# Performance work log

Hardware: AMD Instinct MI355X
Metric: run time of the kernel (lower is better)

The kernel has to match this reference:

```python
import jax, jax.numpy as jnp
import numpy as np

V, E, H, L = 32000, 256, 512, 2
B, T, S = 64, 64, 64


def setup_inputs() -> dict:
    key = jax.random.key(0)
    ks = jax.random.split(key, 20)
    p = lambda k, shape: (0.02 * jax.random.normal(k, shape)).astype(jnp.float32)
    return {
        "X": jax.random.randint(ks[0], (B, T), 0, V),
        "enc_outputs": jax.random.normal(ks[1], (B, S, H), dtype=jnp.float32),
        "hidden_state": jax.random.normal(ks[2], (L, B, H), dtype=jnp.float32),
        "enc_valid_lens": jax.random.randint(ks[3], (B,), 1, S + 1),
        "emb": p(ks[4], (V, E)),
        "Wq": p(ks[5], (H, H)),
        "Wk": p(ks[6], (H, H)),
        "wv": p(ks[7], (H,)),
        "W_ih0": p(ks[8], (3 * H, E + H)),
        "W_hh0": p(ks[9], (3 * H, H)),
        "b_ih0": p(ks[10], (3 * H,)),
        "b_hh0": p(ks[11], (3 * H,)),
        "W_ih1": p(ks[12], (3 * H, H)),
        "W_hh1": p(ks[13], (3 * H, H)),
        "b_ih1": p(ks[14], (3 * H,)),
        "b_hh1": p(ks[15], (3 * H,)),
        "dense_W": p(ks[16], (V, H)),
        "dense_b": p(ks[17], (V,)),
    }


def _gru_cell(x, h, W_ih, W_hh, b_ih, b_hh):
    gi = x @ W_ih.T + b_ih            # [B, 3H]
    gh = h @ W_hh.T + b_hh            # [B, 3H]
    i_r, i_z, i_n = jnp.split(gi, 3, axis=-1)
    h_r, h_z, h_n = jnp.split(gh, 3, axis=-1)
    r = jax.nn.sigmoid(i_r + h_r)
    z = jax.nn.sigmoid(i_z + h_z)
    n = jnp.tanh(i_n + r * h_n)
    return (1.0 - z) * n + z * h


def reference(X, enc_outputs, hidden_state, enc_valid_lens, emb, Wq, Wk, wv,
              W_ih0, W_hh0, b_ih0, b_hh0, W_ih1, W_hh1, b_ih1, b_hh1,
              dense_W, dense_b):
    # token embeddings, time-major: [T, B, E]
    x_seq = jnp.transpose(emb[X], (1, 0, 2))
    keys_proj = jnp.einsum('bsh,kh->bsk', enc_outputs, Wk)  # precompute W_k(K)
    valid_mask = jnp.arange(S)[None, :] < enc_valid_lens[:, None]  # [B, S]

    def step(h, x_t):
        q = h[-1] @ Wq.T                                     # [B, H]
        feat = jnp.tanh(q[:, None, :] + keys_proj)           # [B, S, H]
        scores = feat @ wv                                   # [B, S]
        attn = jax.nn.softmax(jnp.where(valid_mask, scores, -1e6), axis=-1)
        context = jnp.einsum('bs,bsh->bh', attn, enc_outputs)
        inp = jnp.concatenate([context, x_t], axis=-1)       # [B, H+E]
        h0 = _gru_cell(inp, h[0], W_ih0, W_hh0, b_ih0, b_hh0)
        h1 = _gru_cell(h0, h[1], W_ih1, W_hh1, b_ih1, b_hh1)
        return jnp.stack([h0, h1]), h1

    h_final, outs = jax.lax.scan(step, hidden_state, x_seq)  # outs: [T, B, H]
    logits = outs @ dense_W.T + dense_b                      # [T, B, V]
    return jnp.transpose(logits, (1, 0, 2))                  # [B, T, V]
```

## Files before the change

### kernel.cpp

```cpp
#include <hip/hip_runtime.h>
#include <hip/hip_bf16.h>
#include <hip/hip_fp16.h>

#define VV 32000
#define EE 256
#define HH 512
#define BB 64
#define TT 64
#define SS 64
#define G3 1536
#define NGRU 256
#define STU 16384

typedef __attribute__((ext_vector_type(8))) short bf16x8;
typedef __attribute__((ext_vector_type(4))) float f32x4;
typedef _Float16 half2v __attribute__((ext_vector_type(2)));

__device__ __forceinline__ half2v bch(unsigned u) { return __builtin_bit_cast(half2v, u); }

__device__ __forceinline__ void async16(void* lds, const void* g) {
  __builtin_amdgcn_global_load_lds((const __attribute__((address_space(1))) void*)g,
                                   (__attribute__((address_space(3))) void*)lds, 16, 0, 0);
}

__device__ __forceinline__ float sigmoid_fast(float x) {
  return 1.0f / (1.0f + __expf(-x));
}
__device__ __forceinline__ float tanh_fast(float x) {
  x = fminf(fmaxf(x, -15.f), 15.f);
  float e = __expf(2.f * x);
  return (e - 1.f) / (e + 1.f);
}
__device__ __forceinline__ float2 unpackh2(unsigned u) {
  __half2 h = *reinterpret_cast<__half2*>(&u);
  return __half22float2(h);
}
__device__ __forceinline__ unsigned packh2(float x, float y) {
  __half2 h = __floats2half2_rn(x, y);
  return *reinterpret_cast<unsigned*>(&h);
}
__device__ __forceinline__ unsigned packh2w(float x, float y) {
  half2v h; h[0] = (_Float16)x; h[1] = (_Float16)y;
  return __builtin_bit_cast(unsigned, h);
}

__device__ __forceinline__ void stg_sc(float* p, float v) {
  asm volatile("global_store_dword %0, %1, off sc0 sc1" :: "v"(p), "v"(v) : "memory");
}
__device__ __forceinline__ void stg_scu(unsigned* p, unsigned v) {
  asm volatile("global_store_dword %0, %1, off sc0 sc1" :: "v"(p), "v"(v) : "memory");
}
__device__ __forceinline__ void stg_scu2(unsigned* p, uint2 v) {
  asm volatile("global_store_dwordx2 %0, %1, off sc0 sc1" :: "v"(p), "v"(v) : "memory");
}
__device__ __forceinline__ void stg_sci(int* p, int v) {
  asm volatile("global_store_dword %0, %1, off sc0 sc1" :: "v"(p), "v"(v) : "memory");
}
__device__ __forceinline__ int ld_agent(const int* p) {
  return __hip_atomic_load(p, __ATOMIC_RELAXED, __HIP_MEMORY_SCOPE_AGENT);
}

template <int NBK>
__device__ __forceinline__ void gbar(int* flags, int* go, int phase) {
  __syncthreads();
  if (blockIdx.x == NBK - 1) {
    if (threadIdx.x < 64) {
      const int l = threadIdx.x;
      if (l == 0) stg_sci(&flags[NBK - 1], phase);
      for (;;) {
        bool ok = true;
#pragma unroll
        for (int g = 0; g < NBK / 64; ++g) ok &= (ld_agent(&flags[l + 64 * g]) >= phase);
        if (__all(ok)) break;
        __builtin_amdgcn_s_sleep(1);
      }
      if (l == 0) stg_sci(go, phase);
    }
  } else {
    if (threadIdx.x == 0) {
      stg_sci(&flags[blockIdx.x], phase);
      while (ld_agent(go) < phase) __builtin_amdgcn_s_sleep(1);
    }
  }
  __syncthreads();
}

__global__ __launch_bounds__(256) void transpose_kernel(float* __restrict__ dst,
                                                        const float* __restrict__ src,
                                                        int R, int C, int ld, int off) {
  __shared__ float tile[32][33];
  int c0 = blockIdx.x * 32, r0 = blockIdx.y * 32;
  int x = threadIdx.x, y = threadIdx.y;
  for (int i = y; i < 32; i += 8) tile[i][x] = src[(size_t)(r0 + i) * ld + off + c0 + x];
  __syncthreads();
  for (int i = y; i < 32; i += 8) dst[(size_t)(c0 + i) * R + r0 + x] = tile[x][i];
}

__global__ __launch_bounds__(256) void cast_kernel(const float* __restrict__ src,
                                                   __hip_bfloat16* __restrict__ dst, int n) {
  for (int i = blockIdx.x * blockDim.x + threadIdx.x; i < n; i += gridDim.x * blockDim.x)
    dst[i] = __float2bfloat16(src[i]);
}

__global__ __launch_bounds__(256) void hspack_kernel(const float* __restrict__ hs,
                                                     unsigned* __restrict__ h0u,
                                                     unsigned* __restrict__ h1u) {
  int i = blockIdx.x * 256 + threadIdx.x;
  int layer = i >> 14, r = i & 16383;
  int b = r >> 8, kp = r & 255;
  const float* src = hs + (size_t)layer * BB * HH + (size_t)b * HH + 2 * kp;
  unsigned u = packh2(src[0], src[1]);
  (layer ? h1u : h0u)[(kp >> 1) * 128 + 2 * b + (kp & 1)] = u;
}

__global__ __launch_bounds__(256) void gemm32_kernel(const float* __restrict__ A,
                                                     const int* __restrict__ Xtb,
                                                     const float* __restrict__ Bk,
                                                     const float* __restrict__ bias,
                                                     float* __restrict__ C,
                                                     int N, int K, int ldb, int tbmaj) {
  __shared__ float Xs[32][65];
  __shared__ float Ws[32][129];
  __shared__ int toks[64];
  int m0 = blockIdx.x * 64, n0 = blockIdx.y * 128;
  int tid = threadIdx.x;
  if (tid < 64) {
    int m = m0 + tid;
    toks[tid] = Xtb ? Xtb[(m & 63) * TT + (m >> 6)] : m;
  }
  __syncthreads();
  float acc[4][8];
#pragma unroll
  for (int i = 0; i < 4; ++i)
#pragma unroll
    for (int j = 0; j < 8; ++j) acc[i][j] = 0.f;
  int mi = (tid >> 4) * 4;
  int ni = (tid & 15) * 8;
  for (int kc = 0; kc < K; kc += 32) {
#pragma unroll
    for (int i = 0; i < 16; ++i) {
      int idx = tid + i * 256;
      int kk = idx >> 7, nn = idx & 127;
      Ws[kk][nn] = Bk[(size_t)(kc + kk) * ldb + n0 + nn];
    }
#pragma unroll
    for (int i = 0; i < 8; ++i) {
      int idx = tid + i * 256;
      int mm = idx >> 5, kk = idx & 31;
      Xs[kk][mm] = A[(size_t)toks[mm] * K + kc + kk];
    }
    __syncthreads();
#pragma unroll
    for (int k = 0; k < 32; ++k) {
      float xv[4], wv[8];
#pragma unroll
      for (int i = 0; i < 4; ++i) xv[i] = Xs[k][mi + i];
#pragma unroll
      for (int j = 0; j < 8; ++j) wv[j] = Ws[k][ni + j];
#pragma unroll
      for (int i = 0; i < 4; ++i)
#pragma unroll
        for (int j = 0; j < 8; ++j) acc[i][j] += xv[i] * wv[j];
    }
    __syncthreads();
  }
#pragma unroll
  for (int i = 0; i < 4; ++i) {
    int m = m0 + mi + i;
#pragma unroll
    for (int j = 0; j < 8; ++j) {
      int n = n0 + ni + j;
      float v = acc[i][j] + (bias ? bias[n] : 0.f);
      if (tbmaj) C[((size_t)(m >> 6) * N + n) * BB + (m & 63)] = v;
      else       C[(size_t)m * N + n] = v;
    }
  }
}

struct RecArgs {
  const float *Wq, *W_ih0, *W_hh0, *W_ih1, *W_hh1;
  const float *b_hh0, *b_ih1, *b_hh1;
  const float *gixT, *keysp, *enc, *wv;
  const int* vlen;
  const unsigned *h0i, *h1i;
  float *qS;
  unsigned *ctxS, *h0S, *h1S;
  int *flags, *go;
  __hip_bfloat16* outsb;
};

__device__ __forceinline__ void accum6(const unsigned* __restrict__ xu, int xkp0,
                                       const unsigned (*__restrict__ WL)[8], int wkp0,
                                       int nkp, int b, float s[6]) {
#pragma unroll 4
  for (int i = 0; i < nkp; i += 2) {
    uint2 xv = *(const uint2*)(xu + ((xkp0 + i) >> 1) * 128 + 2 * b);
    half2v x0 = bch(xv.x), x1 = bch(xv.y);
    const unsigned* w0 = WL[wkp0 + i];
    const unsigned* w1 = WL[wkp0 + i + 1];
#pragma unroll
    for (int g = 0; g < 6; ++g) {
      s[g] = __builtin_amdgcn_fdot2(bch(w0[g]), x0, s[g], false);
      s[g] = __builtin_amdgcn_fdot2(bch(w1[g]), x1, s[g], false);
    }
  }
}

template <bool HOIST, int NBK>
__global__ __launch_bounds__(512, 4) void recurrent_kernel(RecArgs a) {
  const int blk = blockIdx.x, tid = threadIdx.x;
  const int w = tid >> 6, lane = tid & 63;
  const bool isGru = HOIST ? (blk < NGRU) : true;
  const bool isAttn = HOIST ? (blk >= NGRU) : (blk < BB);
  const int battn = HOIST ? (blk - NGRU) : blk;
  const int j0 = 2 * blk;

  __shared__ __align__(16) unsigned WLh[2][512][8];
  __shared__ __align__(16) unsigned QLh[256][2];
  __shared__ float redW[6][8][64];
  __shared__ float redH0s[6][64], redH1s[6][64];
  __shared__ float sQ[HH], sWV[HH], sCt[HH], sAttn[SS];

  if (isGru) {
    for (int idx = tid; idx < 2 * 3072; idx += 512) {
      int layer = idx / 3072;
      int rem = idx - layer * 3072;
      int kp = rem / 6, g = rem - kp * 6;
      int gate = g >> 1, jj = g & 1;
      int row = gate * 512 + j0 + jj;
      float w0, w1;
      if (layer == 0) {
        if (kp < 256) { w0 = a.W_ih0[(size_t)row * 768 + 2 * kp];
                        w1 = a.W_ih0[(size_t)row * 768 + 2 * kp + 1]; }
        else          { w0 = a.W_hh0[(size_t)row * 512 + 2 * (kp - 256)];
                        w1 = a.W_hh0[(size_t)row * 512 + 2 * (kp - 256) + 1]; }
      } else {
        if (kp < 256) { w0 = a.W_ih1[(size_t)row * 512 + 2 * kp];
                        w1 = a.W_ih1[(size_t)row * 512 + 2 * kp + 1]; }
        else          { w0 = a.W_hh1[(size_t)row * 512 + 2 * (kp - 256)];
                        w1 = a.W_hh1[(size_t)row * 512 + 2 * (kp - 256) + 1]; }
      }
      WLh[layer][kp][g] = packh2w(w0, w1);
    }
    {
      int kp = tid >> 1, jj = tid & 1;
      QLh[kp][jj] = packh2w(a.Wq[(size_t)(j0 + jj) * HH + 2 * kp],
                            a.Wq[(size_t)(j0 + jj) * HH + 2 * kp + 1]);
    }
  }
  if (isAttn) sWV[tid] = a.wv[tid];
  const int vl = isAttn ? a.vlen[battn] : 0;
  const int hoff = isGru ? ((blk >> 1) * 128 + (blk & 1)) : 0;
  __syncthreads();

  for (int t = 0; t < TT; ++t) {
    const unsigned* h0p = (t == 0) ? a.h0i : a.h0S + (size_t)(t - 1) * STU;
    const unsigned* h1p = (t == 0) ? a.h1i : a.h1S + (size_t)(t - 1) * STU;
    float* qrowT = a.qS + (size_t)t * BB * HH;
    unsigned* ctxu = a.ctxS + (size_t)t * STU;
    unsigned* h0n  = a.h0S + (size_t)t * STU;
    unsigned* h1n  = a.h1S + (size_t)t * STU;

    if (isGru) {
      float q0 = 0.f, q1 = 0.f;
      const int kp0 = w * 32;
#pragma unroll 4
      for (int i = 0; i < 32; i += 2) {
        uint2 xv = *(const uint2*)(h1p + ((kp0 + i) >> 1) * 128 + 2 * lane);
        half2v x0 = bch(xv.x), x1 = bch(xv.y);
        q0 = __builtin_amdgcn_fdot2(bch(QLh[kp0 + i][0]), x0, q0, false);
        q0 = __builtin_amdgcn_fdot2(bch(QLh[kp0 + i + 1][0]), x1, q0, false);
        q1 = __builtin_amdgcn_fdot2(bch(QLh[kp0 + i][1]), x0, q1, false);
        q1 = __builtin_amdgcn_fdot2(bch(QLh[kp0 + i + 1][1]), x1, q1, false);
      }
      redW[0][w][lane] = q0; redW[1][w][lane] = q1;
      __syncthreads();
      if (tid < 64) {
        int b = tid;
        float v0 = 0.f, v1 = 0.f;
#pragma unroll
        for (int q = 0; q < 8; ++q) { v0 += redW[0][q][b]; v1 += redW[1][q][b]; }
        stg_sc(&qrowT[(size_t)b * HH + j0], v0);
        stg_sc(&qrowT[(size_t)b * HH + j0 + 1], v1);
      }
    }
    gbar<NBK>(a.flags, a.go, t * 4 + 1);

    if (HOIST && isGru) {
      float s[6] = {0, 0, 0, 0, 0, 0};
      const int layer = (w >= 4) ? 1 : 0;
      const unsigned* xp = layer ? h1p : h0p;
      const int c = (w & 3) * 64;
      accum6(xp, c, WLh[layer], 256 + c, 64, lane, s);
#pragma unroll
      for (int g = 0; g < 6; ++g) redW[g][w][lane] = s[g];
      __syncthreads();
      if (tid < 128) {
        int b = tid & 63, jj = tid >> 6;
#pragma unroll
        for (int g = 0; g < 3; ++g) {
          int sl = 2 * g + jj;
          redH0s[sl][b] = redW[sl][0][b] + redW[sl][1][b] + redW[sl][2][b] + redW[sl][3][b];
          redH1s[sl][b] = redW[sl][4][b] + redW[sl][5][b] + redW[sl][6][b] + redW[sl][7][b];
        }
      }
    } else if (isAttn) {
      const int b = battn;
      sQ[tid] = qrowT[(size_t)b * HH + tid];
      __syncthreads();
      for (int s = w; s < SS; s += 8) {
        const float* kp = a.keysp + ((size_t)b * SS + s) * HH;
        float p = 0.f;
#pragma unroll
        for (int h = lane; h < HH; h += 64)
          p += tanh_fast(sQ[h] + kp[h]) * sWV[h];
#pragma unroll
        for (int off = 32; off > 0; off >>= 1) p += __shfl_down(p, off);
        if (lane == 0) sAttn[s] = (s < vl) ? p : -1e6f;
      }
      __syncthreads();
      if (w == 0) {
        float v = sAttn[lane];
        float mx = v;
        for (int off = 32; off > 0; off >>= 1) mx = fmaxf(mx, __shfl_xor(mx, off));
        float e = __expf(v - mx);
        float sm = e;
        for (int off = 32; off > 0; off >>= 1) sm += __shfl_xor(sm, off);
        sAttn[lane] = e / sm;
      }
      __syncthreads();
      {
        float c = 0.f;
#pragma unroll 8
        for (int s = 0; s < SS; ++s) c += sAttn[s] * a.enc[((size_t)b * SS + s) * HH + tid];
        sCt[tid] = c;
      }
      __syncthreads();
      if (tid < 128) {
        uint2 v;
        v.x = packh2(sCt[4 * tid], sCt[4 * tid + 1]);
        v.y = packh2(sCt[4 * tid + 2], sCt[4 * tid + 3]);
        stg_scu2(&ctxu[tid * 128 + 2 * b], v);
      }
    }
    gbar<NBK>(a.flags, a.go, t * 4 + 2);

    if (isGru) {
      float gr0, gz0, gn0, gr1, gz1, gn1;
      unsigned holdu = 0;
      if (tid < 64) {
        const int b = tid;
        const float* gx = a.gixT + (size_t)t * G3 * BB;
        gr0 = gx[(size_t)(j0)*BB + b];          gr1 = gx[(size_t)(j0 + 1) * BB + b];
        gz0 = gx[(size_t)(j0 + 512) * BB + b];  gz1 = gx[(size_t)(j0 + 513) * BB + b];
        gn0 = gx[(size_t)(j0 + 1024) * BB + b]; gn1 = gx[(size_t)(j0 + 1025) * BB + b];
        holdu = h0p[hoff + 2 * b];
      }
      float s[6] = {0, 0, 0, 0, 0, 0};
      if (HOIST) {
        accum6(ctxu, w * 32, WLh[0], w * 32, 32, lane, s);
      } else {
        const int c = (w & 3) * 64;
        if (w < 4) accum6(ctxu, c, WLh[0], c, 64, lane, s);
        else       accum6(h0p,  c, WLh[0], 256 + c, 64, lane, s);
      }
#pragma unroll
      for (int g = 0; g < 6; ++g) redW[g][w][lane] = s[g];
      __syncthreads();
      if (tid < 64) {
        const int b = tid;
        float2 hold = unpackh2(holdu);
        float hv[2];
#pragma unroll
        for (int jj = 0; jj < 2; ++jj) {
          int j = j0 + jj;
          float Ri = 0, Zi = 0, Ni = 0, Rh = 0, Zh = 0, Nh = 0;
          if (HOIST) {
#pragma unroll
            for (int q = 0; q < 8; ++q) {
              Ri += redW[jj][q][b]; Zi += redW[2 + jj][q][b]; Ni += redW[4 + jj][q][b];
            }
            Rh = redH0s[jj][b]; Zh = redH0s[2 + jj][b]; Nh = redH0s[4 + jj][b];
          } else {
#pragma unroll
            for (int q = 0; q < 4; ++q) {
              Ri += redW[jj][q][b];     Rh += redW[jj][4 + q][b];
              Zi += redW[2 + jj][q][b]; Zh += redW[2 + jj][4 + q][b];
              Ni += redW[4 + jj][q][b]; Nh += redW[4 + jj][4 + q][b];
            }
          }
          float gr = jj ? gr1 : gr0, gz = jj ? gz1 : gz0, gn = jj ? gn1 : gn0;
          float r = sigmoid_fast(gr + Ri + a.b_hh0[j] + Rh);
          float z = sigmoid_fast(gz + Zi + a.b_hh0[j + 512] + Zh);
          float n = tanh_fast(gn + Ni + r * (a.b_hh0[j + 1024] + Nh));
          float ho = jj ? hold.y : hold.x;
          hv[jj] = (1.f - z) * n + z * ho;
        }
        stg_scu(&h0n[hoff + 2 * b], packh2(hv[0], hv[1]));
      }
    }
    gbar<NBK>(a.flags, a.go, t * 4 + 3);

    if (isGru) {
      unsigned holdu = 0;
      if (tid < 64) holdu = h1p[hoff + 2 * tid];
      float s[6] = {0, 0, 0, 0, 0, 0};
      if (HOIST) {
        accum6(h0n, w * 32, WLh[1], w * 32, 32, lane, s);
      } else {
        const int c = (w & 3) * 64;
        if (w < 4) accum6(h0n, c, WLh[1], c, 64, lane, s);
        else       accum6(h1p, c, WLh[1], 256 + c, 64, lane, s);
      }
#pragma unroll
      for (int g = 0; g < 6; ++g) redW[g][w][lane] = s[g];
      __syncthreads();
      if (tid < 64) {
        const int b = tid;
        float2 hold = unpackh2(holdu);
        float hv[2];
#pragma unroll
        for (int jj = 0; jj < 2; ++jj) {
          int j = j0 + jj;
          float Ri = 0, Zi = 0, Ni = 0, Rh = 0, Zh = 0, Nh = 0;
          if (HOIST) {
#pragma unroll
            for (int q = 0; q < 8; ++q) {
              Ri += redW[jj][q][b]; Zi += redW[2 + jj][q][b]; Ni += redW[4 + jj][q][b];
            }
            Rh = redH1s[jj][b]; Zh = redH1s[2 + jj][b]; Nh = redH1s[4 + jj][b];
          } else {
#pragma unroll
            for (int q = 0; q < 4; ++q) {
              Ri += redW[jj][q][b];     Rh += redW[jj][4 + q][b];
              Zi += redW[2 + jj][q][b]; Zh += redW[2 + jj][4 + q][b];
              Ni += redW[4 + jj][q][b]; Nh += redW[4 + jj][4 + q][b];
            }
          }
          float r = sigmoid_fast(a.b_ih1[j] + Ri + a.b_hh1[j] + Rh);
          float z = sigmoid_fast(a.b_ih1[j + 512] + Zi + a.b_hh1[j + 512] + Zh);
          float n = tanh_fast(a.b_ih1[j + 1024] + Ni + r * (a.b_hh1[j + 1024] + Nh));
          float ho = jj ? hold.y : hold.x;
          hv[jj] = (1.f - z) * n + z * ho;
          a.outsb[((size_t)t * BB + b) * HH + j] = __float2bfloat16(hv[jj]);
        }
        stg_scu(&h1n[hoff + 2 * b], packh2(hv[0], hv[1]));
      }
    }
    gbar<NBK>(a.flags, a.go, t * 4 + 4);
  }
}

__global__ __launch_bounds__(256) void dense_kernel(const __hip_bfloat16* __restrict__ A,
                                                    const __hip_bfloat16* __restrict__ Bt,
                                                    const float* __restrict__ bias,
                                                    float* __restrict__ out) {
  __shared__ __align__(16) short As[128 * 64];
  __shared__ __align__(16) short Bs[128 * 64];
  int mt = blockIdx.x;
  int nt = blockIdx.y;
  int tid = threadIdx.x;
  int w = tid >> 6, lane = tid & 63;
  int wm = w >> 1, wn = w & 1;
  f32x4 acc[4][4];
#pragma unroll
  for (int m = 0; m < 4; ++m)
#pragma unroll
    for (int n = 0; n < 4; ++n) acc[m][n] = (f32x4)0.f;

  const short* Ag = (const short*)A + (size_t)(mt * 128) * 512;
  const short* Bg = (const short*)Bt + (size_t)(nt * 128) * 512;

  for (int kt = 0; kt < 8; ++kt) {
    int k0 = kt * 64;
#pragma unroll
    for (int c = 0; c < 4; ++c) {
      int chunk = w * 4 + c;
      int row = chunk * 8 + (lane >> 3);
      int col = (lane & 7) * 8;
      async16(As + chunk * 512, Ag + (size_t)row * 512 + k0 + col);
      async16(Bs + chunk * 512, Bg + (size_t)row * 512 + k0 + col);
    }
    __syncthreads();
#pragma unroll
    for (int kk = 0; kk < 2; ++kk) {
      int krow = kk * 32 + (lane >> 4) * 8;
      bf16x8 af[4], bf[4];
#pragma unroll
      for (int m = 0; m < 4; ++m) {
        int r = wm * 64 + m * 16 + (lane & 15);
        af[m] = *(const bf16x8*)&As[r * 64 + krow];
      }
#pragma unroll
      for (int n = 0; n < 4; ++n) {
        int r = wn * 64 + n * 16 + (lane & 15);
        bf[n] = *(const bf16x8*)&Bs[r * 64 + krow];
      }
#pragma unroll
      for (int m = 0; m < 4; ++m)
#pragma unroll
        for (int n = 0; n < 4; ++n)
          acc[m][n] = __builtin_amdgcn_mfma_f32_16x16x32_bf16(af[m], bf[n], acc[m][n], 0, 0, 0);
    }
    __syncthreads();
  }
#pragma unroll
  for (int m = 0; m < 4; ++m) {
    int rbase = mt * 128 + wm * 64 + m * 16 + (lane >> 4) * 4;
#pragma unroll
    for (int n = 0; n < 4; ++n) {
      int v = nt * 128 + wn * 64 + n * 16 + (lane & 15);
      float bv = bias[v];
#pragma unroll
      for (int r = 0; r < 4; ++r) {
        int mi = rbase + r;
        size_t off = (size_t)(mi & 63) * (TT * VV) + (size_t)(mi >> 6) * VV + v;
        out[off] = acc[m][n][r] + bv;
      }
    }
  }
}

extern "C" void kernel_launch(void* const* d_in, const int* in_sizes, int n_in,
                              void* d_out, int out_size, void* d_ws, size_t ws_size,
                              hipStream_t stream) {
  const int*   X     = (const int*)d_in[0];
  const float* enc   = (const float*)d_in[1];
  const float* hs    = (const float*)d_in[2];
  const int*   vlen  = (const int*)d_in[3];
  const float* emb   = (const float*)d_in[4];
  const float* Wq    = (const float*)d_in[5];
  const float* Wk    = (const float*)d_in[6];
  const float* wv    = (const float*)d_in[7];
  const float* W_ih0 = (const float*)d_in[8];
  const float* W_hh0 = (const float*)d_in[9];
  const float* b_ih0 = (const float*)d_in[10];
  const float* b_hh0 = (const float*)d_in[11];
  const float* W_ih1 = (const float*)d_in[12];
  const float* W_hh1 = (const float*)d_in[13];
  const float* b_ih1 = (const float*)d_in[14];
  const float* b_hh1 = (const float*)d_in[15];
  const float* dW    = (const float*)d_in[16];
  const float* db    = (const float*)d_in[17];
  float* out = (float*)d_out;

  char* wp = (char*)d_ws;
  auto alloc = [&](size_t bytes) { char* p = wp; wp += (bytes + 255) & ~(size_t)255; return p; };
  __hip_bfloat16* dWb   = (__hip_bfloat16*)alloc((size_t)VV * HH * 2);
  __hip_bfloat16* outsb = (__hip_bfloat16*)alloc((size_t)TT * BB * HH * 2);
  float* keysp = (float*)alloc((size_t)BB * SS * HH * 4);
  float* gixT  = (float*)alloc((size_t)TT * G3 * BB * 4);
  float* WkT   = (float*)alloc((size_t)HH * HH * 4);
  float* WT0e  = (float*)alloc((size_t)EE * G3 * 4);
  float* qS    = (float*)alloc((size_t)TT * BB * HH * 4);
  unsigned* h0i  = (unsigned*)alloc((size_t)STU * 4);
  unsigned* h1i  = (unsigned*)alloc((size_t)STU * 4);
  unsigned* ctxS = (unsigned*)alloc((size_t)TT * STU * 4);
  unsigned* h0S  = (unsigned*)alloc((size_t)TT * STU * 4);
  unsigned* h1S  = (unsigned*)alloc((size_t)TT * STU * 4);
  int* flags = (int*)alloc(320 * sizeof(int));
  int* go    = (int*)alloc(64 * sizeof(int));

  hipMemsetAsync(flags, 0, 320 * sizeof(int), stream);
  hipMemsetAsync(go, 0, 64 * sizeof(int), stream);

  dim3 tb(32, 8);
  transpose_kernel<<<dim3(HH / 32, HH / 32), tb, 0, stream>>>(WkT, Wk, HH, HH, HH, 0);
  transpose_kernel<<<dim3(EE / 32, G3 / 32), tb, 0, stream>>>(WT0e, W_ih0, G3, EE, HH + EE, HH);
  cast_kernel<<<2048, 256, 0, stream>>>(dW, dWb, VV * HH);
  hspack_kernel<<<128, 256, 0, stream>>>(hs, h0i, h1i);

  gemm32_kernel<<<dim3(BB * SS / 64, HH / 128), 256, 0, stream>>>(
      enc, nullptr, WkT, nullptr, keysp, HH, HH, HH, 0);
  gemm32_kernel<<<dim3(TT * BB / 64, G3 / 128), 256, 0, stream>>>(
      emb, X, WT0e, b_ih0, gixT, G3, EE, G3, 1);

  RecArgs args;
  args.Wq = Wq; args.W_ih0 = W_ih0; args.W_hh0 = W_hh0; args.W_ih1 = W_ih1; args.W_hh1 = W_hh1;
  args.b_hh0 = b_hh0; args.b_ih1 = b_ih1; args.b_hh1 = b_hh1;
  args.gixT = gixT; args.keysp = keysp; args.enc = enc; args.wv = wv; args.vlen = vlen;
  args.h0i = h0i; args.h1i = h1i;
  args.qS = qS; args.ctxS = ctxS; args.h0S = h0S; args.h1S = h1S;
  args.flags = flags; args.go = go; args.outsb = outsb;
  void* kp[] = {&args};

  int maxb = 0;
  hipError_t qe = hipOccupancyMaxActiveBlocksPerMultiprocessor(
      &maxb, reinterpret_cast<const void*>(recurrent_kernel<true, 320>), 512, 0);
  bool launchedA = false;
  if (qe == hipSuccess && maxb >= 2) {
    hipError_t le = hipLaunchCooperativeKernel(
        reinterpret_cast<void*>(recurrent_kernel<true, 320>),
        dim3(320), dim3(512), kp, 0, stream);
    launchedA = (le == hipSuccess);
  }
  if (!launchedA) {
    hipLaunchCooperativeKernel(
        reinterpret_cast<void*>(recurrent_kernel<false, 256>),
        dim3(256), dim3(512), kp, 0, stream);
  }

  dense_kernel<<<dim3(32, 250), 256, 0, stream>>>(outsb, dWb, db, out);
}
```

Baseline: 2.229 ms.

## Decentralize grid barrier and pack attention keys/encoder outputs to fp16

The grid barrier no longer relays through a master block writing a go flag. Every block now polls all arrival flags directly, removing one global-memory round trip per barrier at the cost of more polling traffic. Separately, the projected keys and the encoder outputs are pre-packed into half2 words by a new kernel. The per-step attention score and context loops then read half the bytes, with some loss of precision on these activations.

```diff
diff --git a/kernel.cpp b/kernel.cpp
--- a/kernel.cpp
+++ b/kernel.cpp
@@ -61,25 +61,17 @@
 }
 
 template <int NBK>
-__device__ __forceinline__ void gbar(int* flags, int* go, int phase) {
+__device__ __forceinline__ void gbar(int* flags, int phase) {
   __syncthreads();
-  if (blockIdx.x == NBK - 1) {
-    if (threadIdx.x < 64) {
-      const int l = threadIdx.x;
-      if (l == 0) stg_sci(&flags[NBK - 1], phase);
-      for (;;) {
-        bool ok = true;
-#pragma unroll
-        for (int g = 0; g < NBK / 64; ++g) ok &= (ld_agent(&flags[l + 64 * g]) >= phase);
-        if (__all(ok)) break;
-        __builtin_amdgcn_s_sleep(1);
-      }
-      if (l == 0) stg_sci(go, phase);
-    }
-  } else {
-    if (threadIdx.x == 0) {
-      stg_sci(&flags[blockIdx.x], phase);
-      while (ld_agent(go) < phase) __builtin_amdgcn_s_sleep(1);
+  if (threadIdx.x < 64) {
+    const int l = threadIdx.x;
+    if (l == 0) stg_sci(&flags[blockIdx.x], phase);
+    for (;;) {
+      bool ok = true;
+#pragma unroll
+      for (int g = 0; g < NBK / 64; ++g) ok &= (ld_agent(&flags[l + 64 * g]) >= phase);
+      if (__all(ok)) break;
+      __builtin_amdgcn_s_sleep(1);
     }
   }
   __syncthreads();
@@ -100,6 +92,12 @@
                                                    __hip_bfloat16* __restrict__ dst, int n) {
   for (int i = blockIdx.x * blockDim.x + threadIdx.x; i < n; i += gridDim.x * blockDim.x)
     dst[i] = __float2bfloat16(src[i]);
+}
+
+__global__ __launch_bounds__(256) void packhalf_kernel(const float* __restrict__ src,
+                                                       unsigned* __restrict__ dst, int npairs) {
+  for (int i = blockIdx.x * blockDim.x + threadIdx.x; i < npairs; i += gridDim.x * blockDim.x)
+    dst[i] = packh2(src[2 * i], src[2 * i + 1]);
 }
 
 __global__ __launch_bounds__(256) void hspack_kernel(const float* __restrict__ hs,
@@ -180,12 +178,13 @@
 struct RecArgs {
   const float *Wq, *W_ih0, *W_hh0, *W_ih1, *W_hh1;
   const float *b_hh0, *b_ih1, *b_hh1;
-  const float *gixT, *keysp, *enc, *wv;
+  const float *gixT, *wv;
+  const unsigned *keysph, *ench;
   const int* vlen;
   const unsigned *h0i, *h1i;
   float *qS;
   unsigned *ctxS, *h0S, *h1S;
-  int *flags, *go;
+  int *flags;
   __hip_bfloat16* outsb;
 };
 
@@ -284,7 +283,7 @@
         stg_sc(&qrowT[(size_t)b * HH + j0 + 1], v1);
       }
     }
-    gbar<NBK>(a.flags, a.go, t * 4 + 1);
+    gbar<NBK>(a.flags, t * 4 + 1);
 
     if (HOIST && isGru) {
       float s[6] = {0, 0, 0, 0, 0, 0};
@@ -309,11 +308,15 @@
       sQ[tid] = qrowT[(size_t)b * HH + tid];
       __syncthreads();
       for (int s = w; s < SS; s += 8) {
-        const float* kp = a.keysp + ((size_t)b * SS + s) * HH;
+        const unsigned* kp = a.keysph + ((size_t)b * SS + s) * 256;
         float p = 0.f;
 #pragma unroll
-        for (int h = lane; h < HH; h += 64)
-          p += tanh_fast(sQ[h] + kp[h]) * sWV[h];
+        for (int i = 0; i < 4; ++i) {
+          int hp = lane + 64 * i;
+          float2 kv = unpackh2(kp[hp]);
+          p += tanh_fast(sQ[2 * hp] + kv.x) * sWV[2 * hp]
+             + tanh_fast(sQ[2 * hp + 1] + kv.y) * sWV[2 * hp + 1];
+        }
 #pragma unroll
         for (int off = 32; off > 0; off >>= 1) p += __shfl_down(p, off);
         if (lane == 0) sAttn[s] = (s < vl) ? p : -1e6f;
@@ -329,11 +332,16 @@
         sAttn[lane] = e / sm;
       }
       __syncthreads();
-      {
-        float c = 0.f;
+      if (tid < 256) {
+        float c0 = 0.f, c1 = 0.f;
+        const unsigned* ep = a.ench + (size_t)b * SS * 256 + tid;
 #pragma unroll 8
-        for (int s = 0; s < SS; ++s) c += sAttn[s] * a.enc[((size_t)b * SS + s) * HH + tid];
-        sCt[tid] = c;
+        for (int s = 0; s < SS; ++s) {
+          float at = sAttn[s];
+          float2 ev = unpackh2(ep[s * 256]);
+          c0 += at * ev.x; c1 += at * ev.y;
+        }
+        sCt[2 * tid] = c0; sCt[2 * tid + 1] = c1;
       }
       __syncthreads();
       if (tid < 128) {
@@ -343,7 +351,7 @@
         stg_scu2(&ctxu[tid * 128 + 2 * b], v);
       }
     }
-    gbar<NBK>(a.flags, a.go, t * 4 + 2);
+    gbar<NBK>(a.flags, t * 4 + 2);
 
     if (isGru) {
       float gr0, gz0, gn0, gr1, gz1, gn1;
@@ -399,7 +407,7 @@
         stg_scu(&h0n[hoff + 2 * b], packh2(hv[0], hv[1]));
       }
     }
-    gbar<NBK>(a.flags, a.go, t * 4 + 3);
+    gbar<NBK>(a.flags, t * 4 + 3);
 
     if (isGru) {
       unsigned holdu = 0;
@@ -447,7 +455,7 @@
         stg_scu(&h1n[hoff + 2 * b], packh2(hv[0], hv[1]));
       }
     }
-    gbar<NBK>(a.flags, a.go, t * 4 + 4);
+    gbar<NBK>(a.flags, t * 4 + 4);
   }
 }
 
@@ -553,16 +561,16 @@
   float* WkT   = (float*)alloc((size_t)HH * HH * 4);
   float* WT0e  = (float*)alloc((size_t)EE * G3 * 4);
   float* qS    = (float*)alloc((size_t)TT * BB * HH * 4);
+  unsigned* keysph = (unsigned*)alloc((size_t)BB * SS * 256 * 4);
+  unsigned* ench   = (unsigned*)alloc((size_t)BB * SS * 256 * 4);
   unsigned* h0i  = (unsigned*)alloc((size_t)STU * 4);
   unsigned* h1i  = (unsigned*)alloc((size_t)STU * 4);
   unsigned* ctxS = (unsigned*)alloc((size_t)TT * STU * 4);
   unsigned* h0S  = (unsigned*)alloc((size_t)TT * STU * 4);
   unsigned* h1S  = (unsigned*)alloc((size_t)TT * STU * 4);
   int* flags = (int*)alloc(320 * sizeof(int));
-  int* go    = (int*)alloc(64 * sizeof(int));
 
   hipMemsetAsync(flags, 0, 320 * sizeof(int), stream);
-  hipMemsetAsync(go, 0, 64 * sizeof(int), stream);
 
   dim3 tb(32, 8);
   transpose_kernel<<<dim3(HH / 32, HH / 32), tb, 0, stream>>>(WkT, Wk, HH, HH, HH, 0);
@@ -574,14 +582,16 @@
       enc, nullptr, WkT, nullptr, keysp, HH, HH, HH, 0);
   gemm32_kernel<<<dim3(TT * BB / 64, G3 / 128), 256, 0, stream>>>(
       emb, X, WT0e, b_ih0, gixT, G3, EE, G3, 1);
+  packhalf_kernel<<<1024, 256, 0, stream>>>(keysp, keysph, BB * SS * 256);
+  packhalf_kernel<<<1024, 256, 0, stream>>>(enc, ench, BB * SS * 256);
 
   RecArgs args;
   args.Wq = Wq; args.W_ih0 = W_ih0; args.W_hh0 = W_hh0; args.W_ih1 = W_ih1; args.W_hh1 = W_hh1;
   args.b_hh0 = b_hh0; args.b_ih1 = b_ih1; args.b_hh1 = b_hh1;
-  args.gixT = gixT; args.keysp = keysp; args.enc = enc; args.wv = wv; args.vlen = vlen;
+  args.gixT = gixT; args.wv = wv; args.keysph = keysph; args.ench = ench; args.vlen = vlen;
   args.h0i = h0i; args.h1i = h1i;
   args.qS = qS; args.ctxS = ctxS; args.h0S = h0S; args.h1S = h1S;
-  args.flags = flags; args.go = go; args.outsb = outsb;
+  args.flags = flags; args.outsb = outsb;
   void* kp[] = {&args};
 
   int maxb = 0;
```

New measurement: 2.851 ms. 1.28x slower.
